# Optimization experiments

Measured on AMD Instinct MI355X. Metric: run time of the kernel, lower is better.

Reference implementation:

```python
import jax, jax.numpy as jnp
import numpy as np

B, T, C = 2, 2048, 1024
H = 16
D = C // H
E = 16
K = 2
THETA = 10000.0
ALPHA = 0.01
EPS = 1e-5


def rmsnorm(x, w):
    ms = jnp.mean(jnp.square(x), axis=-1, keepdims=True)
    return x * jax.lax.rsqrt(ms + EPS) * w


def rope_cos_sin(t_len, dim):
    # matches precompute_freqs_cis: freqs = theta**(-2i/dim), angles = t * freqs
    freqs = 1.0 / THETA ** (jnp.arange(0, dim // 2, dtype=jnp.float32) * 2.0 / dim)
    ang = jnp.arange(t_len, dtype=jnp.float32)[:, None] * freqs[None, :]  # [T, D/2]
    return jnp.cos(ang), jnp.sin(ang)


def apply_rope(x, cos, sin):
    # x: [B,T,H,D]; complex rotation on consecutive pairs (view_as_complex semantics)
    xr = x.reshape(x.shape[:-1] + (D // 2, 2))
    x0, x1 = xr[..., 0], xr[..., 1]
    c = cos[None, :, None, :]
    s = sin[None, :, None, :]
    return jnp.stack([x0 * c - x1 * s, x0 * s + x1 * c], axis=-1).reshape(x.shape)


def mlp(x, wf, bf, wp, bp):
    return jax.nn.silu(x @ wf + bf) @ wp + bp


def setup_inputs() -> dict:
    key = jax.random.key(0)
    ks = jax.random.split(key, 16)
    s = 0.02
    return {
        'x': jax.random.normal(ks[0], (B, T, C), jnp.float32),
        'ln1_w': jax.random.normal(ks[1], (C,), jnp.float32),
        'ln2_w': jax.random.normal(ks[2], (C,), jnp.float32),
        'w_attn': jax.random.normal(ks[3], (C, 3 * C), jnp.float32) * s,
        'b_attn': jnp.zeros((3 * C,), jnp.float32),
        'w_proj': jax.random.normal(ks[4], (C, C), jnp.float32) * s,
        'b_proj': jnp.zeros((C,), jnp.float32),
        'gate_w': jax.random.normal(ks[5], (E, C), jnp.float32) * s,
        'gate_bias': jnp.zeros((E,), jnp.float32),
        'exp_wf': jax.random.normal(ks[6], (E, C, 2 * C), jnp.float32) * s,
        'exp_bf': jnp.zeros((E, 2 * C), jnp.float32),
        'exp_wp': jax.random.normal(ks[7], (E, 2 * C, C), jnp.float32) * s,
        'exp_bp': jnp.zeros((E, C), jnp.float32),
        'sh_wf': jax.random.normal(ks[8], (C, 2 * C), jnp.float32) * s,
        'sh_bf': jnp.zeros((2 * C,), jnp.float32),
        'sh_wp': jax.random.normal(ks[9], (2 * C, C), jnp.float32) * s,
        'sh_bp': jnp.zeros((C,), jnp.float32),
    }


def reference(x, ln1_w, ln2_w, w_attn, b_attn, w_proj, b_proj, gate_w, gate_bias,
              exp_wf, exp_bf, exp_wp, exp_bp, sh_wf, sh_bf, sh_wp, sh_bp):
    # ---- attention sub-block ----
    h = rmsnorm(x, ln1_w)
    qkv = h @ w_attn + b_attn  # [B,T,3C]
    q, k, v = jnp.split(qkv, 3, axis=-1)
    q = q.reshape(B, T, H, D)
    k = k.reshape(B, T, H, D)
    v = v.reshape(B, T, H, D)
    cos, sin = rope_cos_sin(T, D)
    q = apply_rope(q, cos, sin)
    k = apply_rope(k, cos, sin)
    scores = jnp.einsum('bqhd,bkhd->bhqk', q, k) / jnp.sqrt(jnp.float32(D))
    causal = jnp.tril(jnp.ones((T, T), dtype=bool))
    scores = jnp.where(causal, scores, -jnp.inf)
    attn = jax.nn.softmax(scores, axis=-1)
    y = jnp.einsum('bhqk,bkhd->bqhd', attn, v).reshape(B, T, C)
    x = x + y @ w_proj + b_proj
    # ---- MoE sub-block ----
    h = rmsnorm(x, ln2_w).reshape(-1, C)  # [N,C]
    N = h.shape[0]
    logits = h @ gate_w.T
    p = jax.nn.softmax(logits.astype(jnp.float32), axis=-1)  # original_scores [N,E]
    _, idx = jax.lax.top_k(p + gate_bias, K)  # topk on biased scores
    w_sel = jnp.take_along_axis(p, idx, axis=-1)  # weights from unbiased scores [N,K]
    onehot = jax.nn.one_hot(idx, E, dtype=p.dtype)  # [N,K,E]
    w_dense = jnp.sum(onehot * w_sel[..., None], axis=1)  # [N,E] combine weights
    counts = jnp.sum(onehot, axis=(0, 1))  # bincount
    f_i = counts * E / (K * N + 1e-6)
    expert_probs = p.mean(axis=0)
    lb_loss = ALPHA * jnp.sum(f_i * expert_probs)
    out = jnp.zeros_like(h)
    for i in range(E):  # fixed small expert count
        out = out + mlp(h, exp_wf[i], exp_bf[i], exp_wp[i], exp_bp[i]) * w_dense[:, i:i + 1]
    out = out + mlp(h, sh_wf, sh_bf, sh_wp, sh_bp)
    return x + out.reshape(B, T, C), lb_loss
```

## Files before the change

### kernel.cpp

```cpp
#include <hip/hip_runtime.h>

typedef __bf16 bf16x8 __attribute__((ext_vector_type(8)));
typedef short  short8 __attribute__((ext_vector_type(8)));
typedef float  f32x4  __attribute__((ext_vector_type(4)));
typedef unsigned short u16;

#define NTOK 4096
#define TSEQ 2048
#define CDIM 1024
#define NEXP 16

__device__ __forceinline__ u16 f2bf(float f){
  union { float f; unsigned u; } v; v.f = f;
  unsigned r = v.u + 0x7fffu + ((v.u >> 16) & 1u);
  return (u16)(r >> 16);
}

__device__ __forceinline__ f32x4 mfma16(short8 a, short8 b, f32x4 c){
  return __builtin_amdgcn_mfma_f32_16x16x32_bf16(
      __builtin_bit_cast(bf16x8, a), __builtin_bit_cast(bf16x8, b), c, 0, 0, 0);
}

__device__ __forceinline__ void gload_lds16(const void* g, void* l){
  __builtin_amdgcn_global_load_lds((__attribute__((address_space(1))) void*)g,
                                   (__attribute__((address_space(3))) void*)l,
                                   16, 0, 0);
}

__global__ void transpose_all_k(const float* __restrict__ wAttn, const float* __restrict__ wProj,
                                const float* __restrict__ shWf,  const float* __restrict__ shWp,
                                const float* __restrict__ expWf, const float* __restrict__ expWp,
                                u16* __restrict__ oAttn, u16* __restrict__ oProj,
                                u16* __restrict__ oWf17, u16* __restrict__ oWp17)
{
  int bid = blockIdx.x;
  const float* in; u16* out; int K, N, k0, n0;
  if (bid < 8192) {
    int z = bid >> 9, r = bid & 511;
    in = expWf + (size_t)z * 2048 * 1024; out = oWf17 + (size_t)z * 2048 * 1024;
    K = 1024; N = 2048; n0 = (r & 31) * 64; k0 = (r >> 5) * 64;
  } else if (bid < 16384) {
    int z = (bid - 8192) >> 9, r = (bid - 8192) & 511;
    in = expWp + (size_t)z * 2048 * 1024; out = oWp17 + (size_t)z * 2048 * 1024;
    K = 2048; N = 1024; n0 = (r & 15) * 64; k0 = (r >> 4) * 64;
  } else if (bid < 17152) {
    int r = bid - 16384;
    in = wAttn; out = oAttn; K = 1024; N = 3072; n0 = (r % 48) * 64; k0 = (r / 48) * 64;
  } else if (bid < 17664) {
    int r = bid - 17152;
    in = shWf; out = oWf17 + (size_t)16 * 2048 * 1024;
    K = 1024; N = 2048; n0 = (r & 31) * 64; k0 = (r >> 5) * 64;
  } else if (bid < 18176) {
    int r = bid - 17664;
    in = shWp; out = oWp17 + (size_t)16 * 2048 * 1024;
    K = 2048; N = 1024; n0 = (r & 15) * 64; k0 = (r >> 4) * 64;
  } else {
    int r = bid - 18176;
    in = wProj; out = oProj; K = 1024; N = 1024; n0 = (r & 15) * 64; k0 = (r >> 4) * 64;
  }

  __shared__ u16 lds16[64 * 66];
  int tid = threadIdx.x;
  int tx = tid & 15;
#pragma unroll
  for (int p = 0; p < 2; ++p) {
    int q = (tid >> 4) + p * 16;
    int k = 2 * q;
    float4 v0 = *(const float4*)(in + (size_t)(k0 + k)     * N + n0 + tx * 4);
    float4 v1 = *(const float4*)(in + (size_t)(k0 + k + 1) * N + n0 + tx * 4);
    const float* a0 = (const float*)&v0;
    const float* a1 = (const float*)&v1;
#pragma unroll
    for (int i = 0; i < 4; ++i) {
      unsigned val = (unsigned)f2bf(a0[i]) | ((unsigned)f2bf(a1[i]) << 16);
      *(unsigned*)&lds16[(tx * 4 + i) * 66 + k] = val;
    }
  }
  __syncthreads();
#pragma unroll
  for (int p = 0; p < 2; ++p) {
    int n = (tid >> 3) + p * 32;
    int k8 = (tid & 7) * 8;
    const unsigned* l32 = (const unsigned*)&lds16[n * 66 + k8];
    uint4 o4;
    o4.x = l32[0]; o4.y = l32[1]; o4.z = l32[2]; o4.w = l32[3];
    *(uint4*)(out + (size_t)(n0 + n) * K + k0 + k8) = o4;
  }
}

__global__ void rmsnorm_k(const float* __restrict__ x, const float* __restrict__ w,
                          u16* __restrict__ ob, float* __restrict__ of)
{
  int row = blockIdx.x, tid = threadIdx.x;
  const float4* xr = (const float4*)(x + (size_t)row * CDIM);
  float4 v = xr[tid];
  float ss = v.x*v.x + v.y*v.y + v.z*v.z + v.w*v.w;
  for (int d = 1; d < 64; d <<= 1) ss += __shfl_xor(ss, d);
  __shared__ float wacc[4];
  if ((tid & 63) == 0) wacc[tid >> 6] = ss;
  __syncthreads();
  float tot = wacc[0] + wacc[1] + wacc[2] + wacc[3];
  float scale = rsqrtf(tot * (1.0f / CDIM) + 1e-5f);
  float4 wv = ((const float4*)w)[tid];
  float o0 = v.x * scale * wv.x, o1 = v.y * scale * wv.y;
  float o2 = v.z * scale * wv.z, o3 = v.w * scale * wv.w;
  if (of) ((float4*)(of + (size_t)row * CDIM))[tid] = make_float4(o0, o1, o2, o3);
  ushort4 ov; ov.x = f2bf(o0); ov.y = f2bf(o1); ov.z = f2bf(o2); ov.w = f2bf(o3);
  ((ushort4*)(ob + (size_t)row * CDIM))[tid] = ov;
}

template<int MODE>
__global__ void __launch_bounds__(256, 4)
gemm_bt(const u16* __restrict__ A, int lda,
        const u16* __restrict__ Bt, long long bStrideZ,
        const float* __restrict__ bias, int biasStrideZ,
        void* __restrict__ Cout,
        const float* __restrict__ resid,
        int M, int N, int K,
        const int* __restrict__ counts, const int* __restrict__ offsets,
        const int* __restrict__ tokA)
{
  int nwg = gridDim.x * gridDim.y * gridDim.z;
  int d = (blockIdx.z * gridDim.y + blockIdx.y) * gridDim.x + blockIdx.x;
  int o = (d & 7) * (nwg >> 3) + (d >> 3);
  int cb = o % gridDim.x;
  int t2 = o / gridDim.x;
  int rb = t2 % gridDim.y;
  int z  = t2 / gridDim.y;

  int mLoc = M, rowBase = 0;
  if (counts) { mLoc = counts[z]; rowBase = offsets[z]; }
  if (rb * 128 >= mLoc) return;

  const u16* Bz = Bt + (size_t)z * bStrideZ;
  const float* bz = bias + (size_t)z * biasStrideZ;

  __shared__ u16 lds_a[2][128 * 32];
  __shared__ u16 lds_b[2][128 * 32];

  int tid = threadIdx.x;
  int lane = tid & 63, wave = tid >> 6;
  int wm = wave >> 1, wn = wave & 1;
  int srow = wave * 16 + (lane >> 2);
  int skel = (lane & 3) * 8;
  int r16 = lane & 15, g8 = (lane >> 4) * 8;

  size_t arow[2];
  int ncol[2];
#pragma unroll
  for (int c = 0; c < 2; ++c) {
    int rloc = rb * 128 + c * 64 + srow;
    if (rloc >= mLoc) rloc = mLoc - 1;
    int grow = rowBase + rloc;
    arow[c] = tokA ? (size_t)tokA[grow] : (size_t)grow;
    ncol[c] = cb * 128 + c * 64 + srow;
  }

  f32x4 acc[4][4] = {};

  auto stage = [&](int kt, int buf){
    int k0 = kt * 32;
#pragma unroll
    for (int c = 0; c < 2; ++c) {
      gload_lds16(A + arow[c] * lda + k0 + skel,
                  (char*)&lds_a[buf][0] + c * 4096 + wave * 1024);
      gload_lds16(Bz + (size_t)ncol[c] * K + k0 + skel,
                  (char*)&lds_b[buf][0] + c * 4096 + wave * 1024);
    }
  };

  int nkt = K >> 5;
  stage(0, 0);
  for (int kt = 0; kt < nkt; ++kt) {
    int buf = kt & 1;
    if (kt + 1 < nkt) {
      stage(kt + 1, buf ^ 1);
      asm volatile("s_waitcnt vmcnt(4)" ::: "memory");
    } else {
      asm volatile("s_waitcnt vmcnt(0)" ::: "memory");
    }
    __builtin_amdgcn_s_barrier();
    short8 af[4], bfr[4];
#pragma unroll
    for (int i = 0; i < 4; ++i) {
      af[i]  = *(const short8*)&lds_a[buf][(wm * 64 + i * 16 + r16) * 32 + g8];
      bfr[i] = *(const short8*)&lds_b[buf][(wn * 64 + i * 16 + r16) * 32 + g8];
    }
#pragma unroll
    for (int i = 0; i < 4; ++i)
#pragma unroll
      for (int j = 0; j < 4; ++j)
        acc[i][j] = mfma16(af[i], bfr[j], acc[i][j]);
    __builtin_amdgcn_s_barrier();
  }

#pragma unroll
  for (int i = 0; i < 4; ++i) {
    int rl0 = rb * 128 + wm * 64 + i * 16 + (lane >> 4) * 4;
#pragma unroll
    for (int j = 0; j < 4; ++j) {
      int col = cb * 128 + wn * 64 + j * 16 + r16;
      float bv = bz[col];
#pragma unroll
      for (int r = 0; r < 4; ++r) {
        int rl = rl0 + r;
        if (rl >= mLoc) continue;
        int grow = rowBase + rl;
        float v = acc[i][j][r] + bv;
        if (MODE == 0) {
          ((float*)Cout)[(size_t)grow * N + col] = v;
        } else if (MODE == 1) {
          ((float*)Cout)[(size_t)grow * N + col] = v + resid[(size_t)grow * N + col];
        } else {
          float s = v * (1.0f / (1.0f + __expf(-v)));
          ((u16*)Cout)[(size_t)grow * N + col] = f2bf(s);
        }
      }
    }
  }
}

__global__ void rope_split_k(const float* __restrict__ qkv,
                             u16* __restrict__ qr, u16* __restrict__ kr,
                             u16* __restrict__ vt)
{
  int flat = blockIdx.x * 256 + threadIdx.x;
  int i = flat & 31;
  int h = (flat >> 5) & 15;
  int n = flat >> 9;
  int b = n >> 11, t = n & 2047;
  const float* row = qkv + (size_t)n * 3072;
  float2 q = *(const float2*)(row + h * 64 + 2 * i);
  float2 k = *(const float2*)(row + 1024 + h * 64 + 2 * i);
  float2 v = *(const float2*)(row + 2048 + h * 64 + 2 * i);
  float freq = expf(-(float)i * (2.0f / 64.0f) * 9.210340371976184f);
  float ang = (float)t * freq;
  float sn, cs;
  sincosf(ang, &sn, &cs);
  float q0 = q.x * cs - q.y * sn, q1 = q.x * sn + q.y * cs;
  float k0 = k.x * cs - k.y * sn, k1 = k.x * sn + k.y * cs;
  int bh = b * 16 + h;
  size_t qoff = ((size_t)bh * TSEQ + t) * 64 + 2 * i;
  *(unsigned*)(qr + qoff) = (unsigned)f2bf(q0) | ((unsigned)f2bf(q1) << 16);
  *(unsigned*)(kr + qoff) = (unsigned)f2bf(k0) | ((unsigned)f2bf(k1) << 16);
  size_t voff = ((size_t)bh * 64 + 2 * i) * TSEQ + t;
  vt[voff] = f2bf(v.x);
  vt[voff + TSEQ] = f2bf(v.y);
}

__global__ void __launch_bounds__(512, 4)
attn_k(const u16* __restrict__ qr, const u16* __restrict__ kr,
       const u16* __restrict__ vt, u16* __restrict__ y)
{
  int bh = blockIdx.y;
  int b = bh >> 4, h = bh & 15;
  int qb = gridDim.x - 1 - blockIdx.x;
  int tid = threadIdx.x;
  int wv = tid >> 6, lane = tid & 63;
  int qrow0 = qb * 128 + wv * 16;
  const u16* qbase = qr + (size_t)bh * TSEQ * 64;
  const u16* kbase = kr + (size_t)bh * TSEQ * 64;
  const u16* vbase = vt + (size_t)bh * 64 * TSEQ;

  __shared__ u16 lK[2][64 * 64];
  __shared__ u16 lV[2][64 * 64];
  __shared__ u16 plds[8][16 * 72];
  u16* pw = &plds[wv][0];

  int r16 = lane & 15, g = lane >> 4;

  short8 aq0 = *(const short8*)(qbase + (size_t)(qrow0 + r16) * 64 + g * 8);
  short8 aq1 = *(const short8*)(qbase + (size_t)(qrow0 + r16) * 64 + 32 + g * 8);

  int sRow = tid >> 3;
  int sColE = (((tid & 7) * 16) ^ ((sRow & 7) << 4)) >> 1;

  float m[4] = {-1e30f, -1e30f, -1e30f, -1e30f};
  float l[4] = {0.f, 0.f, 0.f, 0.f};
  f32x4 o[4] = {};

  int nt = 2 * qb + 2;

  auto stage = [&](int t, int buf){
    int kp = t * 64;
    gload_lds16(kbase + ((size_t)(kp + sRow) << 6) + sColE,
                (char*)&lK[buf][0] + wv * 1024);
    gload_lds16(vbase + (size_t)sRow * TSEQ + kp + sColE,
                (char*)&lV[buf][0] + wv * 1024);
  };

  auto compute = [&](int t, int buf){
    int kp = t * 64;
    f32x4 s[4];
    __builtin_amdgcn_s_setprio(1);
#pragma unroll
    for (int st = 0; st < 4; ++st) {
      int rowK = st * 16 + r16;
      int sw = (rowK & 7) << 4;
      short8 kb0 = *(const short8*)((const char*)&lK[buf][0] + rowK * 128 + ((g * 16) ^ sw));
      short8 kb1 = *(const short8*)((const char*)&lK[buf][0] + rowK * 128 + ((64 + g * 16) ^ sw));
      f32x4 acc = {0.f, 0.f, 0.f, 0.f};
      acc = mfma16(aq0, kb0, acc);
      acc = mfma16(aq1, kb1, acc);
      s[st] = acc;
    }
    __builtin_amdgcn_s_setprio(0);

    float sc[4];
#pragma unroll
    for (int r = 0; r < 4; ++r) {
      int qpos = qrow0 + g * 4 + r;
      float v0 = (kp + r16      <= qpos) ? s[0][r] * 0.125f : -1e30f;
      float v1 = (kp + 16 + r16 <= qpos) ? s[1][r] * 0.125f : -1e30f;
      float v2 = (kp + 32 + r16 <= qpos) ? s[2][r] * 0.125f : -1e30f;
      float v3 = (kp + 48 + r16 <= qpos) ? s[3][r] * 0.125f : -1e30f;
      float mx = fmaxf(fmaxf(v0, v1), fmaxf(v2, v3));
      for (int d = 1; d < 16; d <<= 1) mx = fmaxf(mx, __shfl_xor(mx, d));
      float mnew = fmaxf(m[r], mx);
      float e0 = __expf(v0 - mnew), e1 = __expf(v1 - mnew);
      float e2 = __expf(v2 - mnew), e3 = __expf(v3 - mnew);
      float scale = __expf(m[r] - mnew);
      float rs = (e0 + e1) + (e2 + e3);
      for (int d = 1; d < 16; d <<= 1) rs += __shfl_xor(rs, d);
      l[r] = l[r] * scale + rs;
      m[r] = mnew;
      sc[r] = scale;
      int prow = (g * 4 + r) * 72;
      pw[prow + r16]      = f2bf(e0);
      pw[prow + 16 + r16] = f2bf(e1);
      pw[prow + 32 + r16] = f2bf(e2);
      pw[prow + 48 + r16] = f2bf(e3);
    }
#pragma unroll
    for (int c = 0; c < 4; ++c) {
      f32x4 t4 = o[c];
      t4[0] *= sc[0]; t4[1] *= sc[1]; t4[2] *= sc[2]; t4[3] *= sc[3];
      o[c] = t4;
    }

    short8 pa0 = *(const short8*)&pw[r16 * 72 + g * 8];
    short8 pa1 = *(const short8*)&pw[r16 * 72 + 32 + g * 8];
    __builtin_amdgcn_s_setprio(1);
#pragma unroll
    for (int c = 0; c < 4; ++c) {
      int rowV = c * 16 + r16;
      int sw = (rowV & 7) << 4;
      short8 vb0 = *(const short8*)((const char*)&lV[buf][0] + rowV * 128 + ((g * 16) ^ sw));
      short8 vb1 = *(const short8*)((const char*)&lV[buf][0] + rowV * 128 + ((64 + g * 16) ^ sw));
      o[c] = mfma16(pa0, vb0, o[c]);
      o[c] = mfma16(pa1, vb1, o[c]);
    }
    __builtin_amdgcn_s_setprio(0);
  };

  stage(0, 0);
  for (int t = 0; t < nt; ++t) {
    int buf = t & 1;
    if (t + 1 < nt) {
      stage(t + 1, buf ^ 1);
      asm volatile("s_waitcnt vmcnt(2)" ::: "memory");
    } else {
      asm volatile("s_waitcnt vmcnt(0)" ::: "memory");
    }
    __builtin_amdgcn_s_barrier();
    compute(t, buf);
    __builtin_amdgcn_s_barrier();
  }

#pragma unroll
  for (int c = 0; c < 4; ++c)
#pragma unroll
    for (int r = 0; r < 4; ++r) {
      int qpos = qrow0 + g * 4 + r;
      float val = o[c][r] / l[r];
      y[((size_t)(b * TSEQ + qpos)) * CDIM + h * 64 + c * 16 + r16] = f2bf(val);
    }
}

__global__ void zero_k(int* counts){
  int t = threadIdx.x;
  if (t < NEXP) counts[t] = 0;
}

__global__ void gate_k(const float* __restrict__ h2, const float* __restrict__ gw,
                       const float* __restrict__ gb,
                       int* __restrict__ route_e, float* __restrict__ route_w,
                       int* __restrict__ counts, float* __restrict__ probs)
{
  int n = blockIdx.x, tid = threadIdx.x;
  __shared__ float hrow[CDIM];
  __shared__ float part[16][17];
  __shared__ float sm[16];
  ((float4*)hrow)[tid] = ((const float4*)(h2 + (size_t)n * CDIM))[tid];
  __syncthreads();
  int e = tid & 15, seg = tid >> 4;
  const float4* gw4 = (const float4*)(gw + (size_t)e * CDIM + seg * 64);
  const float4* hs4 = (const float4*)(hrow + seg * 64);
  float p = 0.f;
#pragma unroll
  for (int i = 0; i < 16; ++i) {
    float4 gv = gw4[i];
    float4 hv = hs4[i];
    p += hv.x * gv.x;
    p += hv.y * gv.y;
    p += hv.z * gv.z;
    p += hv.w * gv.w;
  }
  part[e][seg] = p;
  __syncthreads();
  if (tid < 16) {
    float lg = 0.f;
    for (int s = 0; s < 16; ++s) lg += part[tid][s];
    sm[tid] = lg;
  }
  __syncthreads();
  if (tid == 0) {
    float mx = sm[0];
    for (int i = 1; i < 16; ++i) mx = fmaxf(mx, sm[i]);
    float ssum = 0.f;
    for (int i = 0; i < 16; ++i) { float pe = expf(sm[i] - mx); sm[i] = pe; ssum += pe; }
    float inv = 1.0f / ssum;
    for (int i = 0; i < 16; ++i) sm[i] *= inv;
    int i1 = -1; float b1 = -1e30f;
    for (int i = 0; i < 16; ++i) { float t = sm[i] + gb[i]; if (t > b1) { b1 = t; i1 = i; } }
    int i2 = -1; float b2 = -1e30f;
    for (int i = 0; i < 16; ++i) { if (i == i1) continue; float t = sm[i] + gb[i]; if (t > b2) { b2 = t; i2 = i; } }
    route_e[2 * n] = i1; route_e[2 * n + 1] = i2;
    route_w[2 * n] = sm[i1]; route_w[2 * n + 1] = sm[i2];
    atomicAdd(&counts[i1], 1); atomicAdd(&counts[i2], 1);
  }
  __syncthreads();
  if (tid < 16) probs[(size_t)n * 16 + tid] = sm[tid];
}

__global__ void scan_k(const int* counts, int* offs, int* cursors){
  if (threadIdx.x == 0) {
    int acc = 0;
    for (int e = 0; e < NEXP; ++e) { offs[e] = acc; cursors[e] = acc; acc += counts[e]; }
    offs[NEXP] = acc;
  }
}

__global__ void fill_k(const int* __restrict__ route_e, const float* __restrict__ route_w,
                       int* __restrict__ cursors, int* __restrict__ tok, float* __restrict__ tw,
                       int* __restrict__ inv)
{
  int n = blockIdx.x * 256 + threadIdx.x;
  if (n >= NTOK) return;
  for (int j = 0; j < 2; ++j) {
    int e = route_e[2 * n + j];
    int pos = atomicAdd(&cursors[e], 1);
    tok[pos] = n; tw[pos] = route_w[2 * n + j];
    inv[2 * n + j] = pos;
  }
}

__global__ void combine_k(float* __restrict__ out, const float* __restrict__ eout,
                          const int* __restrict__ inv, const float* __restrict__ tw)
{
  int n = blockIdx.x, tid = threadIdx.x;
  int p0 = inv[2 * n], p1 = inv[2 * n + 1];
  float w0 = tw[p0], w1 = tw[p1];
  float4 a  = ((float4*)(out + (size_t)n * CDIM))[tid];
  float4 e0 = ((const float4*)(eout + (size_t)p0 * CDIM))[tid];
  float4 e1 = ((const float4*)(eout + (size_t)p1 * CDIM))[tid];
  a.x += e0.x * w0 + e1.x * w1;
  a.y += e0.y * w0 + e1.y * w1;
  a.z += e0.z * w0 + e1.z * w1;
  a.w += e0.w * w0 + e1.w * w1;
  ((float4*)(out + (size_t)n * CDIM))[tid] = a;
}

__global__ void lb2_k(const int* __restrict__ counts, const float* __restrict__ probs,
                      float* __restrict__ out)
{
  __shared__ float part[256][16];
  int t = threadIdx.x;
  float acc[16];
#pragma unroll
  for (int e = 0; e < 16; ++e) acc[e] = 0.f;
  for (int n = t; n < NTOK; n += 256) {
    const float4* row = (const float4*)(probs + (size_t)n * 16);
    float4 a0 = row[0], a1 = row[1], a2 = row[2], a3 = row[3];
    acc[0] += a0.x; acc[1] += a0.y; acc[2]  += a0.z; acc[3]  += a0.w;
    acc[4] += a1.x; acc[5] += a1.y; acc[6]  += a1.z; acc[7]  += a1.w;
    acc[8] += a2.x; acc[9] += a2.y; acc[10] += a2.z; acc[11] += a2.w;
    acc[12] += a3.x; acc[13] += a3.y; acc[14] += a3.z; acc[15] += a3.w;
  }
#pragma unroll
  for (int e = 0; e < 16; ++e) part[t][e] = acc[e];
  __syncthreads();
  __shared__ float colsum[16];
  if (t < 16) {
    float s = 0.f;
    for (int i = 0; i < 256; ++i) s += part[i][t];
    colsum[t] = s;
  }
  __syncthreads();
  if (t == 0) {
    float accl = 0.f;
    for (int e = 0; e < NEXP; ++e) {
      float f = (float)counts[e] * (16.0f / (2.0f * (float)NTOK + 1e-6f));
      accl += f * (colsum[e] * (1.0f / (float)NTOK));
    }
    out[0] = 0.01f * accl;
  }
}

extern "C" void kernel_launch(void* const* d_in, const int* in_sizes, int n_in,
                              void* d_out, int out_size, void* d_ws, size_t ws_size,
                              hipStream_t stream)
{
  const float* x      = (const float*)d_in[0];
  const float* ln1_w  = (const float*)d_in[1];
  const float* ln2_w  = (const float*)d_in[2];
  const float* w_attn = (const float*)d_in[3];
  const float* b_attn = (const float*)d_in[4];
  const float* w_proj = (const float*)d_in[5];
  const float* b_proj = (const float*)d_in[6];
  const float* gate_w = (const float*)d_in[7];
  const float* gate_b = (const float*)d_in[8];
  const float* exp_wf = (const float*)d_in[9];
  const float* exp_bf = (const float*)d_in[10];
  const float* exp_wp = (const float*)d_in[11];
  const float* exp_bp = (const float*)d_in[12];
  const float* sh_wf  = (const float*)d_in[13];
  const float* sh_bf  = (const float*)d_in[14];
  const float* sh_wp  = (const float*)d_in[15];
  const float* sh_bp  = (const float*)d_in[16];

  char* ws = (char*)d_ws;
  size_t off = 0;
  auto alloc = [&](size_t b){ size_t r = off; off = (off + b + 255) & ~(size_t)255; return r; };

  size_t oWAttnT = alloc(3072ull * 1024 * 2);
  size_t oWProjT = alloc(1024ull * 1024 * 2);
  size_t oExpWfT = alloc(17ull * 2048 * 1024 * 2);
  size_t oExpWpT = alloc(17ull * 1024 * 2048 * 2);
  size_t oX2     = alloc(4096ull * 1024 * 4);
  size_t oH2F    = alloc(4096ull * 2048 * 2);
  size_t oH2B    = alloc(4096ull * 1024 * 2);
  size_t oQKV    = alloc(4096ull * 3072 * 4);
  size_t oQR     = alloc(4096ull * 1024 * 2);
  size_t oKR     = alloc(4096ull * 1024 * 2);
  size_t oVT     = alloc(4096ull * 1024 * 2);
  size_t oH1B    = alloc(4096ull * 1024 * 2);
  size_t oCnt    = alloc(128);
  size_t oOffs   = alloc(128);
  size_t oCurs   = alloc(128);
  size_t oRE     = alloc(8192ull * 4);
  size_t oRW     = alloc(8192ull * 4);
  size_t oTok    = alloc(8192ull * 4);
  size_t oTw     = alloc(8192ull * 4);
  size_t oInv    = alloc(8192ull * 4);
  size_t oProbs  = alloc(4096ull * 16 * 4);

  u16* pWAttnT = (u16*)(ws + oWAttnT);
  u16* pWProjT = (u16*)(ws + oWProjT);
  u16* pWf17   = (u16*)(ws + oExpWfT);
  u16* pWp17   = (u16*)(ws + oExpWpT);
  float* pX2   = (float*)(ws + oX2);
  float* pH2F  = (float*)(ws + oH2F);
  u16* pHidSh  = (u16*)(ws + oH2F);
  u16* pH2B    = (u16*)(ws + oH2B);
  float* pQKV  = (float*)(ws + oQKV);
  u16* pHidMoe = (u16*)(ws + oQKV);
  u16* pQR     = (u16*)(ws + oQR);
  u16* pKR     = (u16*)(ws + oKR);
  u16* pVT     = (u16*)(ws + oVT);
  u16* pH1B    = (u16*)(ws + oH1B);
  u16* pY      = (u16*)(ws + oH1B);
  float* pEout = (float*)(ws + oQR);
  int* pCnt    = (int*)(ws + oCnt);
  int* pOffs   = (int*)(ws + oOffs);
  int* pCurs   = (int*)(ws + oCurs);
  int* pRE     = (int*)(ws + oRE);
  float* pRW   = (float*)(ws + oRW);
  int* pTok    = (int*)(ws + oTok);
  float* pTw   = (float*)(ws + oTw);
  int* pInv    = (int*)(ws + oInv);
  float* pProbs= (float*)(ws + oProbs);

  transpose_all_k<<<18432, 256, 0, stream>>>(w_attn, w_proj, sh_wf, sh_wp, exp_wf, exp_wp,
                                             pWAttnT, pWProjT, pWf17, pWp17);

  rmsnorm_k<<<NTOK, 256, 0, stream>>>(x, ln1_w, pH1B, nullptr);

  gemm_bt<0><<<dim3(3072/128, NTOK/128, 1), 256, 0, stream>>>(
      pH1B, 1024, pWAttnT, 0, b_attn, 0, pQKV, nullptr,
      NTOK, 3072, 1024, nullptr, nullptr, nullptr);

  rope_split_k<<<(NTOK * 16 * 32) / 256, 256, 0, stream>>>(pQKV, pQR, pKR, pVT);

  attn_k<<<dim3(TSEQ/128, 32), 512, 0, stream>>>(pQR, pKR, pVT, pY);

  gemm_bt<1><<<dim3(1024/128, NTOK/128, 1), 256, 0, stream>>>(
      pY, 1024, pWProjT, 0, b_proj, 0, pX2, x,
      NTOK, 1024, 1024, nullptr, nullptr, nullptr);

  rmsnorm_k<<<NTOK, 256, 0, stream>>>(pX2, ln2_w, pH2B, pH2F);

  zero_k<<<1, 64, 0, stream>>>(pCnt);
  gate_k<<<NTOK, 256, 0, stream>>>(pH2F, gate_w, gate_b, pRE, pRW, pCnt, pProbs);
  scan_k<<<1, 64, 0, stream>>>(pCnt, pOffs, pCurs);
  fill_k<<<NTOK/256, 256, 0, stream>>>(pRE, pRW, pCurs, pTok, pTw, pInv);
  lb2_k<<<1, 256, 0, stream>>>(pCnt, pProbs, ((float*)d_out) + (size_t)NTOK * CDIM);

  gemm_bt<2><<<dim3(2048/128, NTOK/128, 1), 256, 0, stream>>>(
      pH2B, 1024, pWf17 + (size_t)16 * 2048 * 1024, 0, sh_bf, 0, pHidSh, nullptr,
      NTOK, 2048, 1024, nullptr, nullptr, nullptr);

  gemm_bt<1><<<dim3(1024/128, NTOK/128, 1), 256, 0, stream>>>(
      pHidSh, 2048, pWp17 + (size_t)16 * 2048 * 1024, 0, sh_bp, 0, (float*)d_out, pX2,
      NTOK, 1024, 2048, nullptr, nullptr, nullptr);

  gemm_bt<2><<<dim3(2048/128, NTOK/128, 16), 256, 0, stream>>>(
      pH2B, 1024, pWf17, 2048ll * 1024, exp_bf, 2048, pHidMoe, nullptr,
      NTOK, 2048, 1024, pCnt, pOffs, pTok);

  gemm_bt<0><<<dim3(1024/128, NTOK/128, 16), 256, 0, stream>>>(
      pHidMoe, 2048, pWp17, 2048ll * 1024, exp_bp, 1024, pEout, nullptr,
      NTOK, 1024, 2048, pCnt, pOffs, nullptr);

  combine_k<<<NTOK, 256, 0, stream>>>((float*)d_out, pEout, pInv, pTw);

  (void)in_sizes; (void)n_in; (void)out_size; (void)ws_size;
}
```

Baseline: 688.9 us.

## Make weight transpose kernel persistent with double-buffered tile prefetch

The weight transpose/convert kernel now runs 2048 blocks, each handling 9 consecutive 64x64 tiles (2048*9 = 18432, the same total as before). Each block loads the next tile's global data into registers while it converts and stores the current one through LDS. The aim is to hide global load latency and cut per-block launch overhead for this large memory-bound kernel. In exchange it uses more registers, adds an extra barrier per tile, and has fewer blocks to spread across CUs.

```diff
diff --git a/kernel.cpp b/kernel.cpp
--- a/kernel.cpp
+++ b/kernel.cpp
@@ -27,14 +27,15 @@
                                    16, 0, 0);
 }
 
-__global__ void transpose_all_k(const float* __restrict__ wAttn, const float* __restrict__ wProj,
-                                const float* __restrict__ shWf,  const float* __restrict__ shWp,
-                                const float* __restrict__ expWf, const float* __restrict__ expWp,
-                                u16* __restrict__ oAttn, u16* __restrict__ oProj,
-                                u16* __restrict__ oWf17, u16* __restrict__ oWp17)
-{
-  int bid = blockIdx.x;
-  const float* in; u16* out; int K, N, k0, n0;
+#define TP_TILES 9
+#define TP_GRID  2048
+
+__device__ __forceinline__ void tp_decode(int bid,
+    const float* wAttn, const float* wProj, const float* shWf, const float* shWp,
+    const float* expWf, const float* expWp,
+    u16* oAttn, u16* oProj, u16* oWf17, u16* oWp17,
+    const float*& in, u16*& out, int& K, int& N, int& k0, int& n0)
+{
   if (bid < 8192) {
     int z = bid >> 9, r = bid & 511;
     in = expWf + (size_t)z * 2048 * 1024; out = oWf17 + (size_t)z * 2048 * 1024;
@@ -58,33 +59,82 @@
     int r = bid - 18176;
     in = wProj; out = oProj; K = 1024; N = 1024; n0 = (r & 15) * 64; k0 = (r >> 4) * 64;
   }
-
+}
+
+__global__ void transpose_all_k(const float* __restrict__ wAttn, const float* __restrict__ wProj,
+                                const float* __restrict__ shWf,  const float* __restrict__ shWp,
+                                const float* __restrict__ expWf, const float* __restrict__ expWp,
+                                u16* __restrict__ oAttn, u16* __restrict__ oProj,
+                                u16* __restrict__ oWf17, u16* __restrict__ oWp17)
+{
   __shared__ u16 lds16[64 * 66];
   int tid = threadIdx.x;
   int tx = tid & 15;
-#pragma unroll
-  for (int p = 0; p < 2; ++p) {
-    int q = (tid >> 4) + p * 16;
-    int k = 2 * q;
-    float4 v0 = *(const float4*)(in + (size_t)(k0 + k)     * N + n0 + tx * 4);
-    float4 v1 = *(const float4*)(in + (size_t)(k0 + k + 1) * N + n0 + tx * 4);
-    const float* a0 = (const float*)&v0;
-    const float* a1 = (const float*)&v1;
-#pragma unroll
-    for (int i = 0; i < 4; ++i) {
-      unsigned val = (unsigned)f2bf(a0[i]) | ((unsigned)f2bf(a1[i]) << 16);
-      *(unsigned*)&lds16[(tx * 4 + i) * 66 + k] = val;
-    }
-  }
-  __syncthreads();
-#pragma unroll
-  for (int p = 0; p < 2; ++p) {
-    int n = (tid >> 3) + p * 32;
-    int k8 = (tid & 7) * 8;
-    const unsigned* l32 = (const unsigned*)&lds16[n * 66 + k8];
-    uint4 o4;
-    o4.x = l32[0]; o4.y = l32[1]; o4.z = l32[2]; o4.w = l32[3];
-    *(uint4*)(out + (size_t)(n0 + n) * K + k0 + k8) = o4;
+  int kq0 = tid >> 4;
+
+  const float *inA, *inB; u16 *outA, *outB;
+  int KA, NA, k0A, n0A, KB, NB, k0B, n0B;
+  float4 vA[4], vB[4];
+
+  auto issue = [&](const float* in, int N, int k0, int n0, float4* v){
+#pragma unroll
+    for (int p = 0; p < 2; ++p) {
+      int k = 2 * (kq0 + p * 16);
+      v[2*p]   = *(const float4*)(in + (size_t)(k0 + k)     * N + n0 + tx * 4);
+      v[2*p+1] = *(const float4*)(in + (size_t)(k0 + k + 1) * N + n0 + tx * 4);
+    }
+  };
+  auto phase1 = [&](const float4* v){
+#pragma unroll
+    for (int p = 0; p < 2; ++p) {
+      int k = 2 * (kq0 + p * 16);
+      const float* a0 = (const float*)&v[2*p];
+      const float* a1 = (const float*)&v[2*p+1];
+#pragma unroll
+      for (int i = 0; i < 4; ++i) {
+        unsigned val = (unsigned)f2bf(a0[i]) | ((unsigned)f2bf(a1[i]) << 16);
+        *(unsigned*)&lds16[(tx * 4 + i) * 66 + k] = val;
+      }
+    }
+  };
+  auto phase2 = [&](u16* out, int K, int k0, int n0){
+#pragma unroll
+    for (int p = 0; p < 2; ++p) {
+      int n = (tid >> 3) + p * 32;
+      int k8 = (tid & 7) * 8;
+      const unsigned* l32 = (const unsigned*)&lds16[n * 66 + k8];
+      uint4 o4;
+      o4.x = l32[0]; o4.y = l32[1]; o4.z = l32[2]; o4.w = l32[3];
+      *(uint4*)(out + (size_t)(n0 + n) * K + k0 + k8) = o4;
+    }
+  };
+
+  int base = blockIdx.x * TP_TILES;
+  tp_decode(base, wAttn, wProj, shWf, shWp, expWf, expWp, oAttn, oProj, oWf17, oWp17,
+            inA, outA, KA, NA, k0A, n0A);
+  issue(inA, NA, k0A, n0A, vA);
+
+#pragma unroll 1
+  for (int i = 0; i < TP_TILES; i += 2) {
+    if (i + 1 < TP_TILES) {
+      tp_decode(base + i + 1, wAttn, wProj, shWf, shWp, expWf, expWp, oAttn, oProj, oWf17, oWp17,
+                inB, outB, KB, NB, k0B, n0B);
+      issue(inB, NB, k0B, n0B, vB);
+    }
+    phase1(vA);
+    __syncthreads();
+    phase2(outA, KA, k0A, n0A);
+    __syncthreads();
+    if (i + 1 >= TP_TILES) break;
+    if (i + 2 < TP_TILES) {
+      tp_decode(base + i + 2, wAttn, wProj, shWf, shWp, expWf, expWp, oAttn, oProj, oWf17, oWp17,
+                inA, outA, KA, NA, k0A, n0A);
+      issue(inA, NA, k0A, n0A, vA);
+    }
+    phase1(vB);
+    __syncthreads();
+    phase2(outB, KB, k0B, n0B);
+    __syncthreads();
   }
 }
 
@@ -581,8 +631,8 @@
   int* pInv    = (int*)(ws + oInv);
   float* pProbs= (float*)(ws + oProbs);
 
-  transpose_all_k<<<18432, 256, 0, stream>>>(w_attn, w_proj, sh_wf, sh_wp, exp_wf, exp_wp,
-                                             pWAttnT, pWProjT, pWf17, pWp17);
+  transpose_all_k<<<TP_GRID, 256, 0, stream>>>(w_attn, w_proj, sh_wf, sh_wp, exp_wf, exp_wp,
+                                               pWAttnT, pWProjT, pWf17, pWp17);
 
   rmsnorm_k<<<NTOK, 256, 0, stream>>>(x, ln1_w, pH1B, nullptr);
 
```

After: 698.1 us. Within noise of the previous version (+1.3%).

## Fuse weight transposes into attention kernel launch to overlap with attention

Applied to the files above, without the earlier changes.

Splits the weight transpose/convert kernel. Only the QKV weight transpose still runs up front. The remaining transposes (proj, shared and expert MLP weights) become extra blocks of the attention kernel, each handling two 64x64 tiles, with LDS shared through a union. The intent is to hide the memory-bound transpose work behind the compute-bound causal attention and remove it from the critical path. The risk is that the transpose blocks compete with attention for CU slots and bandwidth, and that the union raises the LDS footprint seen by the attention blocks.

```diff
diff --git a/kernel.cpp b/kernel.cpp
--- a/kernel.cpp
+++ b/kernel.cpp
@@ -27,40 +27,9 @@
                                    16, 0, 0);
 }
 
-__global__ void transpose_all_k(const float* __restrict__ wAttn, const float* __restrict__ wProj,
-                                const float* __restrict__ shWf,  const float* __restrict__ shWp,
-                                const float* __restrict__ expWf, const float* __restrict__ expWp,
-                                u16* __restrict__ oAttn, u16* __restrict__ oProj,
-                                u16* __restrict__ oWf17, u16* __restrict__ oWp17)
-{
-  int bid = blockIdx.x;
-  const float* in; u16* out; int K, N, k0, n0;
-  if (bid < 8192) {
-    int z = bid >> 9, r = bid & 511;
-    in = expWf + (size_t)z * 2048 * 1024; out = oWf17 + (size_t)z * 2048 * 1024;
-    K = 1024; N = 2048; n0 = (r & 31) * 64; k0 = (r >> 5) * 64;
-  } else if (bid < 16384) {
-    int z = (bid - 8192) >> 9, r = (bid - 8192) & 511;
-    in = expWp + (size_t)z * 2048 * 1024; out = oWp17 + (size_t)z * 2048 * 1024;
-    K = 2048; N = 1024; n0 = (r & 15) * 64; k0 = (r >> 4) * 64;
-  } else if (bid < 17152) {
-    int r = bid - 16384;
-    in = wAttn; out = oAttn; K = 1024; N = 3072; n0 = (r % 48) * 64; k0 = (r / 48) * 64;
-  } else if (bid < 17664) {
-    int r = bid - 17152;
-    in = shWf; out = oWf17 + (size_t)16 * 2048 * 1024;
-    K = 1024; N = 2048; n0 = (r & 31) * 64; k0 = (r >> 5) * 64;
-  } else if (bid < 18176) {
-    int r = bid - 17664;
-    in = shWp; out = oWp17 + (size_t)16 * 2048 * 1024;
-    K = 2048; N = 1024; n0 = (r & 15) * 64; k0 = (r >> 4) * 64;
-  } else {
-    int r = bid - 18176;
-    in = wProj; out = oProj; K = 1024; N = 1024; n0 = (r & 15) * 64; k0 = (r >> 4) * 64;
-  }
-
-  __shared__ u16 lds16[64 * 66];
-  int tid = threadIdx.x;
+__device__ __forceinline__ void tp_body(const float* __restrict__ in, u16* __restrict__ out,
+                                        int K, int N, int k0, int n0, u16* lds16, int tid)
+{
   int tx = tid & 15;
 #pragma unroll
   for (int p = 0; p < 2; ++p) {
@@ -86,6 +55,14 @@
     o4.x = l32[0]; o4.y = l32[1]; o4.z = l32[2]; o4.w = l32[3];
     *(uint4*)(out + (size_t)(n0 + n) * K + k0 + k8) = o4;
   }
+}
+
+__global__ void transpose_wattn_k(const float* __restrict__ in, u16* __restrict__ out)
+{
+  __shared__ u16 lds16[64 * 66];
+  int r = blockIdx.x;
+  int n0 = (r % 48) * 64, k0 = (r / 48) * 64;
+  tp_body(in, out, 1024, 3072, k0, n0, lds16, threadIdx.x);
 }
 
 __global__ void rmsnorm_k(const float* __restrict__ x, const float* __restrict__ w,
@@ -249,12 +226,51 @@
 }
 
 __global__ void __launch_bounds__(512, 4)
-attn_k(const u16* __restrict__ qr, const u16* __restrict__ kr,
-       const u16* __restrict__ vt, u16* __restrict__ y)
-{
-  int bh = blockIdx.y;
+attn_tp_k(const u16* __restrict__ qr, const u16* __restrict__ kr,
+          const u16* __restrict__ vt, u16* __restrict__ y,
+          const float* __restrict__ wProj, const float* __restrict__ shWf,
+          const float* __restrict__ shWp,  const float* __restrict__ expWf,
+          const float* __restrict__ expWp,
+          u16* __restrict__ oProj, u16* __restrict__ oWf17, u16* __restrict__ oWp17)
+{
+  __shared__ union {
+    struct { u16 lK[2][64 * 64]; u16 lV[2][64 * 64]; u16 plds[8][16 * 72]; } a;
+    u16 t[2][64 * 66];
+  } sm;
+
+  int u = blockIdx.x;
+  if (u >= 512) {
+    int tid = threadIdx.x;
+    int half = tid >> 8, t256 = tid & 255;
+    int t = (u - 512) * 2 + half;
+    const float* in; u16* out; int K, N, k0, n0;
+    if (t < 8192) {
+      int z = t >> 9, r = t & 511;
+      in = expWf + (size_t)z * 2048 * 1024; out = oWf17 + (size_t)z * 2048 * 1024;
+      K = 1024; N = 2048; n0 = (r & 31) * 64; k0 = (r >> 5) * 64;
+    } else if (t < 16384) {
+      int z = (t - 8192) >> 9, r = (t - 8192) & 511;
+      in = expWp + (size_t)z * 2048 * 1024; out = oWp17 + (size_t)z * 2048 * 1024;
+      K = 2048; N = 1024; n0 = (r & 15) * 64; k0 = (r >> 4) * 64;
+    } else if (t < 16896) {
+      int r = t - 16384;
+      in = shWf; out = oWf17 + (size_t)16 * 2048 * 1024;
+      K = 1024; N = 2048; n0 = (r & 31) * 64; k0 = (r >> 5) * 64;
+    } else if (t < 17408) {
+      int r = t - 16896;
+      in = shWp; out = oWp17 + (size_t)16 * 2048 * 1024;
+      K = 2048; N = 1024; n0 = (r & 15) * 64; k0 = (r >> 4) * 64;
+    } else {
+      int r = t - 17408;
+      in = wProj; out = oProj; K = 1024; N = 1024; n0 = (r & 15) * 64; k0 = (r >> 4) * 64;
+    }
+    tp_body(in, out, K, N, k0, n0, &sm.t[half][0], t256);
+    return;
+  }
+
+  int bh = u >> 4;
   int b = bh >> 4, h = bh & 15;
-  int qb = gridDim.x - 1 - blockIdx.x;
+  int qb = 15 - (u & 15);
   int tid = threadIdx.x;
   int wv = tid >> 6, lane = tid & 63;
   int qrow0 = qb * 128 + wv * 16;
@@ -262,10 +278,7 @@
   const u16* kbase = kr + (size_t)bh * TSEQ * 64;
   const u16* vbase = vt + (size_t)bh * 64 * TSEQ;
 
-  __shared__ u16 lK[2][64 * 64];
-  __shared__ u16 lV[2][64 * 64];
-  __shared__ u16 plds[8][16 * 72];
-  u16* pw = &plds[wv][0];
+  u16* pw = &sm.a.plds[wv][0];
 
   int r16 = lane & 15, g = lane >> 4;
 
@@ -284,9 +297,9 @@
   auto stage = [&](int t, int buf){
     int kp = t * 64;
     gload_lds16(kbase + ((size_t)(kp + sRow) << 6) + sColE,
-                (char*)&lK[buf][0] + wv * 1024);
+                (char*)&sm.a.lK[buf][0] + wv * 1024);
     gload_lds16(vbase + (size_t)sRow * TSEQ + kp + sColE,
-                (char*)&lV[buf][0] + wv * 1024);
+                (char*)&sm.a.lV[buf][0] + wv * 1024);
   };
 
   auto compute = [&](int t, int buf){
@@ -297,8 +310,8 @@
     for (int st = 0; st < 4; ++st) {
       int rowK = st * 16 + r16;
       int sw = (rowK & 7) << 4;
-      short8 kb0 = *(const short8*)((const char*)&lK[buf][0] + rowK * 128 + ((g * 16) ^ sw));
-      short8 kb1 = *(const short8*)((const char*)&lK[buf][0] + rowK * 128 + ((64 + g * 16) ^ sw));
+      short8 kb0 = *(const short8*)((const char*)&sm.a.lK[buf][0] + rowK * 128 + ((g * 16) ^ sw));
+      short8 kb1 = *(const short8*)((const char*)&sm.a.lK[buf][0] + rowK * 128 + ((64 + g * 16) ^ sw));
       f32x4 acc = {0.f, 0.f, 0.f, 0.f};
       acc = mfma16(aq0, kb0, acc);
       acc = mfma16(aq1, kb1, acc);
@@ -345,8 +358,8 @@
     for (int c = 0; c < 4; ++c) {
       int rowV = c * 16 + r16;
       int sw = (rowV & 7) << 4;
-      short8 vb0 = *(const short8*)((const char*)&lV[buf][0] + rowV * 128 + ((g * 16) ^ sw));
-      short8 vb1 = *(const short8*)((const char*)&lV[buf][0] + rowV * 128 + ((64 + g * 16) ^ sw));
+      short8 vb0 = *(const short8*)((const char*)&sm.a.lV[buf][0] + rowV * 128 + ((g * 16) ^ sw));
+      short8 vb1 = *(const short8*)((const char*)&sm.a.lV[buf][0] + rowV * 128 + ((64 + g * 16) ^ sw));
       o[c] = mfma16(pa0, vb0, o[c]);
       o[c] = mfma16(pa1, vb1, o[c]);
     }
@@ -581,8 +594,7 @@
   int* pInv    = (int*)(ws + oInv);
   float* pProbs= (float*)(ws + oProbs);
 
-  transpose_all_k<<<18432, 256, 0, stream>>>(w_attn, w_proj, sh_wf, sh_wp, exp_wf, exp_wp,
-                                             pWAttnT, pWProjT, pWf17, pWp17);
+  transpose_wattn_k<<<768, 256, 0, stream>>>(w_attn, pWAttnT);
 
   rmsnorm_k<<<NTOK, 256, 0, stream>>>(x, ln1_w, pH1B, nullptr);
 
@@ -592,7 +604,9 @@
 
   rope_split_k<<<(NTOK * 16 * 32) / 256, 256, 0, stream>>>(pQKV, pQR, pKR, pVT);
 
-  attn_k<<<dim3(TSEQ/128, 32), 512, 0, stream>>>(pQR, pKR, pVT, pY);
+  attn_tp_k<<<512 + 8832, 512, 0, stream>>>(pQR, pKR, pVT, pY,
+                                            w_proj, sh_wf, sh_wp, exp_wf, exp_wp,
+                                            pWProjT, pWf17, pWp17);
 
   gemm_bt<1><<<dim3(1024/128, NTOK/128, 1), 256, 0, stream>>>(
       pY, 1024, pWProjT, 0, b_proj, 0, pX2, x,
```

After: 673.3 us. -2.3%, faster.
